# Kernel optimization log

Measured on AMD Instinct MI355X. Metric: run time of the kernel, lower is better.

The kernel has to match this reference:

```python
import jax, jax.numpy as jnp
import numpy as np

N = 50000      # num_nodes
E = 1000000    # graph edges
EP = 400000    # pos/neg link-pred edges
H = 128        # hidden_dim
C = 768        # chemical_dim
L = 2          # num GCN layers


def setup_inputs() -> dict:
    key = jax.random.key(0)
    ks = jax.random.split(key, 12)
    edge_index = jax.random.randint(ks[0], (2, E), 0, N)
    chemistry = jax.random.normal(ks[1], (N, C), jnp.float32)
    pos_edge = jax.random.randint(ks[2], (EP, 2), 0, N)
    neg_edge = jax.random.randint(ks[3], (EP, 2), 0, N)
    smiles_mask = jax.random.uniform(ks[4], (N,), jnp.float32)
    node_emb = jax.random.normal(ks[5], (N, H), jnp.float32) * 0.1
    conv_w = jax.random.normal(ks[6], (L, H, H), jnp.float32) / np.sqrt(H)
    conv_b = jnp.zeros((L, H), jnp.float32)
    chem_w = jax.random.normal(ks[7], (C, H), jnp.float32) / np.sqrt(C)
    chem_b = jnp.zeros((H,), jnp.float32)
    dec_w1 = jax.random.normal(ks[8], (2 * H, H), jnp.float32) / np.sqrt(2 * H)
    dec_b1 = jnp.zeros((H,), jnp.float32)
    dec_w2 = jax.random.normal(ks[9], (H, 1), jnp.float32) / np.sqrt(H)
    dec_b2 = jnp.zeros((1,), jnp.float32)
    return dict(edge_index=edge_index, chemistry=chemistry, pos_edge=pos_edge,
                neg_edge=neg_edge, smiles_mask=smiles_mask, node_emb=node_emb,
                conv_w=conv_w, conv_b=conv_b, chem_w=chem_w, chem_b=chem_b,
                dec_w1=dec_w1, dec_b1=dec_b1, dec_w2=dec_w2, dec_b2=dec_b2)


def reference(edge_index, chemistry, pos_edge, neg_edge, smiles_mask, node_emb,
              conv_w, conv_b, chem_w, chem_b, dec_w1, dec_b1, dec_w2, dec_b2):
    row, col = edge_index[0], edge_index[1]  # src -> dst
    # GCN symmetric normalization (add_self_loops=False)
    deg = jax.ops.segment_sum(jnp.ones((E,), jnp.float32), col, num_segments=N)
    dinv = jnp.where(deg > 0, 1.0 / jnp.sqrt(jnp.maximum(deg, 1.0)), 0.0)
    norm = dinv[row] * dinv[col]  # [E]

    # Encoder: structure-only GCN over learned node embeddings
    z = node_emb
    for l in range(L):
        h = z @ conv_w[l]                       # [N,H]
        msg = h[row] * norm[:, None]            # gather [E,H]
        agg = jax.ops.segment_sum(msg, col, num_segments=N)  # scatter-add
        z = jax.nn.relu(agg + conv_b[l])

    # Chemistry projection, masked by smiles validity
    c = jax.nn.relu(chemistry @ chem_w + chem_b) * smiles_mask[:, None]  # [N,H]

    def decode(edges):
        src, dst = edges[:, 0], edges[:, 1]
        f = jnp.concatenate([z[src] * z[dst], c[src] * c[dst]], axis=-1)  # [Ep,2H]
        hmid = jax.nn.relu(f @ dec_w1 + dec_b1)
        return (hmid @ dec_w2 + dec_b2)[:, 0]

    return decode(pos_edge), decode(neg_edge)
```

## Files before the change

### kernel.cpp

```cpp
#include <hip/hip_runtime.h>
#include <hip/hip_bf16.h>

#define NN 50000
#define NE 1000000
#define NEP 400000
#define HD 128
#define CD 768
#define NB_SCAN 196
#define CKS 24

typedef __attribute__((ext_vector_type(8))) short bf16x8;
typedef __attribute__((ext_vector_type(4))) float f32x4;

__device__ __forceinline__ ushort f2bf(float x) {
    unsigned u = __float_as_uint(x);
    u += 0x7FFF + ((u >> 16) & 1);
    return (ushort)(u >> 16);
}
__device__ __forceinline__ float bf2f(ushort b) {
    return __uint_as_float(((unsigned)b) << 16);
}
__device__ __forceinline__ unsigned pk2bf(float a, float b) {
    __hip_bfloat162 h = __float22bfloat162_rn(make_float2(a, b));
    return *(unsigned*)&h;
}
__device__ __forceinline__ bf16x8 pack8(float4 a0, float4 a1) {
    union { unsigned u[4]; bf16x8 v; } r;
    r.u[0] = pk2bf(a0.x, a0.y);
    r.u[1] = pk2bf(a0.z, a0.w);
    r.u[2] = pk2bf(a1.x, a1.y);
    r.u[3] = pk2bf(a1.z, a1.w);
    return r.v;
}

__global__ __launch_bounds__(256) void count_kernel(const int* __restrict__ col,
                                                    int* __restrict__ cnt) {
    int i = blockIdx.x * 256 + threadIdx.x;
    if (i < NE) atomicAdd(&cnt[col[i]], 1);
}

__global__ __launch_bounds__(256) void dinv_kernel(const int* __restrict__ cnt,
                                                   float* __restrict__ dinv) {
    int i = blockIdx.x * 256 + threadIdx.x;
    if (i < NN) {
        int d = cnt[i];
        dinv[i] = (d > 0) ? 1.0f / sqrtf((float)d) : 0.0f;
    }
}

__global__ __launch_bounds__(256) void scan1_kernel(const int* __restrict__ cnt,
                                                    int* __restrict__ partial,
                                                    int* __restrict__ bsum) {
    __shared__ int s[256];
    int i = blockIdx.x * 256 + threadIdx.x;
    int v = (i < NN) ? cnt[i] : 0;
    s[threadIdx.x] = v;
    __syncthreads();
    for (int o = 1; o < 256; o <<= 1) {
        int t = (threadIdx.x >= o) ? s[threadIdx.x - o] : 0;
        __syncthreads();
        s[threadIdx.x] += t;
        __syncthreads();
    }
    if (i < NN) partial[i] = s[threadIdx.x] - v;
    if (threadIdx.x == 255) bsum[blockIdx.x] = s[255];
}

__global__ __launch_bounds__(256) void scan2_kernel(int* __restrict__ bsum) {
    __shared__ int s[256];
    int v = (threadIdx.x < NB_SCAN) ? bsum[threadIdx.x] : 0;
    s[threadIdx.x] = v;
    __syncthreads();
    for (int o = 1; o < 256; o <<= 1) {
        int t = (threadIdx.x >= o) ? s[threadIdx.x - o] : 0;
        __syncthreads();
        s[threadIdx.x] += t;
        __syncthreads();
    }
    if (threadIdx.x < NB_SCAN) bsum[threadIdx.x] = s[threadIdx.x] - v;
}

__global__ __launch_bounds__(256) void scan3_kernel(const int* __restrict__ partial,
                                                    const int* __restrict__ bsum,
                                                    int* __restrict__ off,
                                                    int* __restrict__ cursor) {
    int i = blockIdx.x * 256 + threadIdx.x;
    if (i < NN) {
        int o = partial[i] + bsum[blockIdx.x];
        off[i] = o;
        cursor[i] = o;
    }
}

__global__ __launch_bounds__(256) void fill_kernel(const int* __restrict__ row,
                                                   const int* __restrict__ col,
                                                   const float* __restrict__ dinv,
                                                   int* __restrict__ cursor,
                                                   int* __restrict__ csr_idx,
                                                   float* __restrict__ csr_w) {
    int e = blockIdx.x * 256 + threadIdx.x;
    if (e < NE) {
        int c = col[e], r = row[e];
        int slot = atomicAdd(&cursor[c], 1);
        csr_idx[slot] = r;
        csr_w[slot] = dinv[r];
    }
}

__global__ __launch_bounds__(256) void wfrag_kernel(const float* __restrict__ w,
                                                    ushort* __restrict__ wf) {
    int tid = blockIdx.x * 256 + threadIdx.x;
    int ks = tid >> 9, nt = (tid >> 6) & 7, l = tid & 63;
    int kbase = ks * 32 + ((l >> 4) << 3);
    int colq = nt * 16 + (l & 15);
    ushort r[8];
#pragma unroll
    for (int j = 0; j < 8; ++j) r[j] = f2bf(w[(size_t)(kbase + j) * HD + colq]);
    *(uint4*)&wf[(size_t)tid * 8] = *(uint4*)r;
}

__global__ __launch_bounds__(256) void matmul_kernel(const float* __restrict__ A,
                                                     const float* __restrict__ W,
                                                     ushort* __restrict__ outb,
                                                     int nrows) {
    __shared__ float Alds[64][64];
    __shared__ float Wlds[64][128];
    const int t = threadIdx.x;
    const int tcol = t & 31, trow = t >> 5;
    const int rowBase = blockIdx.x * 64;

    float4 acc[8];
#pragma unroll
    for (int r = 0; r < 8; ++r) acc[r] = make_float4(0.f, 0.f, 0.f, 0.f);

    for (int kc = 0; kc < HD; kc += 64) {
#pragma unroll
        for (int it = 0; it < 4; ++it) {
            int li = t + it * 256;
            int r = li >> 4, d4 = li & 15;
            int grow = rowBase + r;
            float4 v = make_float4(0.f, 0.f, 0.f, 0.f);
            if (grow < nrows) v = *(const float4*)&A[(size_t)grow * HD + kc + d4 * 4];
            ((float4*)&Alds[0][0])[li] = v;
        }
#pragma unroll
        for (int it = 0; it < 8; ++it) {
            int li = t + it * 256;
            ((float4*)&Wlds[0][0])[li] = ((const float4*)W)[(size_t)kc * 32 + li];
        }
        __syncthreads();
#pragma unroll
        for (int kk = 0; kk < 64; kk += 2) {
            float4 w0 = *(const float4*)&Wlds[kk][tcol * 4];
            float4 w1 = *(const float4*)&Wlds[kk + 1][tcol * 4];
#pragma unroll
            for (int r = 0; r < 8; ++r) {
                float2 a = *(const float2*)&Alds[trow * 8 + r][kk];
                acc[r].x = fmaf(a.x, w0.x, fmaf(a.y, w1.x, acc[r].x));
                acc[r].y = fmaf(a.x, w0.y, fmaf(a.y, w1.y, acc[r].y));
                acc[r].z = fmaf(a.x, w0.z, fmaf(a.y, w1.z, acc[r].z));
                acc[r].w = fmaf(a.x, w0.w, fmaf(a.y, w1.w, acc[r].w));
            }
        }
        __syncthreads();
    }
#pragma unroll
    for (int r = 0; r < 8; ++r) {
        int grow = rowBase + trow * 8 + r;
        if (grow < nrows) {
            uint2 pk;
            pk.x = pk2bf(acc[r].x, acc[r].y);
            pk.y = pk2bf(acc[r].z, acc[r].w);
            *(uint2*)&outb[(size_t)grow * HD + tcol * 4] = pk;
        }
    }
}

__global__ __launch_bounds__(256) void chem_mfma_kernel(const float* __restrict__ chem,
                                                        const ushort* __restrict__ wcf,
                                                        const float* __restrict__ bias,
                                                        const float* __restrict__ mask,
                                                        ushort* __restrict__ cb) {
    __shared__ float At[64][40];
    const int t = threadIdx.x;
    const int w = t >> 6, lane = t & 63;
    const int rowBase = blockIdx.x * 64;
    const int nt0 = w * 2;

    f32x4 acc[4][2] = {};

    for (int ks = 0; ks < CKS; ++ks) {
        __syncthreads();
#pragma unroll
        for (int i = 0; i < 2; ++i) {
            int li = t + i * 256;
            int r = li >> 3, c4 = li & 7;
            int grow = rowBase + r;
            float4 v = make_float4(0.f, 0.f, 0.f, 0.f);
            if (grow < NN) v = *(const float4*)&chem[(size_t)grow * CD + ks * 32 + c4 * 4];
            *(float4*)&At[r][c4 * 4] = v;
        }
        __syncthreads();
        bf16x8 bf0 = ((const bf16x8*)wcf)[(ks * 8 + nt0) * 64 + lane];
        bf16x8 bf1 = ((const bf16x8*)wcf)[(ks * 8 + nt0 + 1) * 64 + lane];
#pragma unroll
        for (int mt = 0; mt < 4; ++mt) {
            int row = mt * 16 + (lane & 15);
            float4 a0 = *(const float4*)&At[row][(lane >> 4) * 8];
            float4 a1 = *(const float4*)&At[row][(lane >> 4) * 8 + 4];
            bf16x8 af = pack8(a0, a1);
            acc[mt][0] = __builtin_amdgcn_mfma_f32_16x16x32_bf16(af, bf0, acc[mt][0], 0, 0, 0);
            acc[mt][1] = __builtin_amdgcn_mfma_f32_16x16x32_bf16(af, bf1, acc[mt][1], 0, 0, 0);
        }
    }

    const int c0 = lane & 15, rq = lane >> 4;
    float bb0 = bias[nt0 * 16 + c0];
    float bb1 = bias[nt0 * 16 + 16 + c0];
#pragma unroll
    for (int mt = 0; mt < 4; ++mt) {
#pragma unroll
        for (int reg = 0; reg < 4; ++reg) {
            int grow = rowBase + mt * 16 + rq * 4 + reg;
            if (grow < NN) {
                float m = mask[grow];
                cb[(size_t)grow * HD + nt0 * 16 + c0] = f2bf(fmaxf(acc[mt][0][reg] + bb0, 0.f) * m);
                cb[(size_t)grow * HD + nt0 * 16 + 16 + c0] = f2bf(fmaxf(acc[mt][1][reg] + bb1, 0.f) * m);
            }
        }
    }
}

template <bool BF16OUT>
__global__ __launch_bounds__(256) void gather_kernel(const int* __restrict__ off,
                                                     const int* __restrict__ cnt,
                                                     const int* __restrict__ csr_idx,
                                                     const float* __restrict__ csr_w,
                                                     const float* __restrict__ dinv,
                                                     const ushort* __restrict__ h,
                                                     const float* __restrict__ bias,
                                                     float* __restrict__ z,
                                                     ushort* __restrict__ zb) {
    int v = blockIdx.x * 4 + (threadIdx.x >> 6);
    if (v >= NN) return;
    int lane = threadIdx.x & 63;
    int s = off[v];
    int e = s + cnt[v];
    float accx = 0.f, accy = 0.f;
    for (; s + 3 < e; s += 4) {
        int r0 = csr_idx[s], r1 = csr_idx[s + 1], r2 = csr_idx[s + 2], r3 = csr_idx[s + 3];
        float w0 = csr_w[s], w1 = csr_w[s + 1], w2 = csr_w[s + 2], w3 = csr_w[s + 3];
        unsigned u0 = *(const unsigned*)&h[(size_t)r0 * HD + lane * 2];
        unsigned u1 = *(const unsigned*)&h[(size_t)r1 * HD + lane * 2];
        unsigned u2 = *(const unsigned*)&h[(size_t)r2 * HD + lane * 2];
        unsigned u3 = *(const unsigned*)&h[(size_t)r3 * HD + lane * 2];
        accx = fmaf(bf2f((ushort)u0), w0, accx); accy = fmaf(bf2f((ushort)(u0 >> 16)), w0, accy);
        accx = fmaf(bf2f((ushort)u1), w1, accx); accy = fmaf(bf2f((ushort)(u1 >> 16)), w1, accy);
        accx = fmaf(bf2f((ushort)u2), w2, accx); accy = fmaf(bf2f((ushort)(u2 >> 16)), w2, accy);
        accx = fmaf(bf2f((ushort)u3), w3, accx); accy = fmaf(bf2f((ushort)(u3 >> 16)), w3, accy);
    }
    for (; s < e; ++s) {
        int r0 = csr_idx[s];
        float w0 = csr_w[s];
        unsigned u0 = *(const unsigned*)&h[(size_t)r0 * HD + lane * 2];
        accx = fmaf(bf2f((ushort)u0), w0, accx); accy = fmaf(bf2f((ushort)(u0 >> 16)), w0, accy);
    }
    float dv = dinv[v];
    float2 b = *(const float2*)&bias[lane * 2];
    float ox = fmaxf(fmaf(accx, dv, b.x), 0.f);
    float oy = fmaxf(fmaf(accy, dv, b.y), 0.f);
    if (BF16OUT) {
        *(unsigned*)&zb[(size_t)v * HD + lane * 2] = pk2bf(ox, oy);
    } else {
        float2 o; o.x = ox; o.y = oy;
        *(float2*)&z[(size_t)v * HD + lane * 2] = o;
    }
}

__global__ __launch_bounds__(256) void decode_mfma_kernel(const int* __restrict__ pos_edge,
                                                          const int* __restrict__ neg_edge,
                                                          const ushort* __restrict__ zb,
                                                          const ushort* __restrict__ cb,
                                                          const ushort* __restrict__ w1f,
                                                          const float* __restrict__ b1,
                                                          const float* __restrict__ w2,
                                                          const float* __restrict__ b2,
                                                          float* __restrict__ out) {
    __shared__ ushort Flds[8 * 4 * 64 * 8];
    __shared__ int sEdge[128];
    __shared__ float part[4][64];
    const int t = threadIdx.x;
    const int w = t >> 6, lane = t & 63;
    const int bid = blockIdx.x;
    const bool isPos = bid < (NEP / 64);
    const int* edges = isPos ? pos_edge : neg_edge;
    const int ebase = (isPos ? bid : bid - NEP / 64) * 64;
    float* op = out + (isPos ? 0 : NEP);

    if (t < 128) sEdge[t] = edges[(size_t)ebase * 2 + t];
    __syncthreads();

    const int seg = lane & 15, esub = lane >> 4;
#pragma unroll
    for (int it = 0; it < 8; ++it) {
        int e = ((it & 3) << 4) | (w << 2) | esub;
        int half = it >> 2;
        const ushort* src = half ? cb : zb;
        int s = sEdge[2 * e], dd = sEdge[2 * e + 1];
        uint4 av = *(const uint4*)&src[(size_t)s * HD + seg * 8];
        uint4 bv = *(const uint4*)&src[(size_t)dd * HD + seg * 8];
        const ushort* ap = (const ushort*)&av;
        const ushort* bp = (const ushort*)&bv;
        uint4 res;
        res.x = pk2bf(bf2f(ap[0]) * bf2f(bp[0]), bf2f(ap[1]) * bf2f(bp[1]));
        res.y = pk2bf(bf2f(ap[2]) * bf2f(bp[2]), bf2f(ap[3]) * bf2f(bp[3]));
        res.z = pk2bf(bf2f(ap[4]) * bf2f(bp[4]), bf2f(ap[5]) * bf2f(bp[5]));
        res.w = pk2bf(bf2f(ap[6]) * bf2f(bp[6]), bf2f(ap[7]) * bf2f(bp[7]));
        int ks = half * 4 + (seg >> 2);
        int mt = it & 3;
        int fl = (e & 15) | ((seg & 3) << 4);
        int idx = (((ks * 4 + mt) * 64) + fl) ^ ((ks & 1) << 2);
        ((uint4*)Flds)[idx] = res;
    }
    __syncthreads();

    f32x4 acc[4][2] = {};
    const int nt0 = w * 2;
#pragma unroll
    for (int ks = 0; ks < 8; ++ks) {
        bf16x8 bf0 = ((const bf16x8*)w1f)[(ks * 8 + nt0) * 64 + lane];
        bf16x8 bf1 = ((const bf16x8*)w1f)[(ks * 8 + nt0 + 1) * 64 + lane];
#pragma unroll
        for (int mt = 0; mt < 4; ++mt) {
            bf16x8 af = ((const bf16x8*)Flds)[((ks * 4 + mt) * 64) + (lane ^ ((ks & 1) << 2))];
            acc[mt][0] = __builtin_amdgcn_mfma_f32_16x16x32_bf16(af, bf0, acc[mt][0], 0, 0, 0);
            acc[mt][1] = __builtin_amdgcn_mfma_f32_16x16x32_bf16(af, bf1, acc[mt][1], 0, 0, 0);
        }
    }

    const int c0 = lane & 15, rq = lane >> 4;
    float b1v0 = b1[nt0 * 16 + c0], b1v1 = b1[nt0 * 16 + 16 + c0];
    float w2v0 = w2[nt0 * 16 + c0], w2v1 = w2[nt0 * 16 + 16 + c0];
#pragma unroll
    for (int mt = 0; mt < 4; ++mt) {
#pragma unroll
        for (int reg = 0; reg < 4; ++reg) {
            float h0 = fmaxf(acc[mt][0][reg] + b1v0, 0.f);
            float h1 = fmaxf(acc[mt][1][reg] + b1v1, 0.f);
            float p = fmaf(h0, w2v0, h1 * w2v1);
            p += __shfl_xor(p, 1);
            p += __shfl_xor(p, 2);
            p += __shfl_xor(p, 4);
            p += __shfl_xor(p, 8);
            if (c0 == 0) part[w][mt * 16 + rq * 4 + reg] = p;
        }
    }
    __syncthreads();
    if (t < 64) {
        op[ebase + t] = part[0][t] + part[1][t] + part[2][t] + part[3][t] + b2[0];
    }
}

extern "C" void kernel_launch(void* const* d_in, const int* in_sizes, int n_in,
                              void* d_out, int out_size, void* d_ws, size_t ws_size,
                              hipStream_t stream) {
    const int* edge_index = (const int*)d_in[0];
    const float* chemistry = (const float*)d_in[1];
    const int* pos_edge = (const int*)d_in[2];
    const int* neg_edge = (const int*)d_in[3];
    const float* smiles_mask = (const float*)d_in[4];
    const float* node_emb = (const float*)d_in[5];
    const float* conv_w = (const float*)d_in[6];
    const float* conv_b = (const float*)d_in[7];
    const float* chem_w = (const float*)d_in[8];
    const float* chem_b = (const float*)d_in[9];
    const float* dec_w1 = (const float*)d_in[10];
    const float* dec_b1 = (const float*)d_in[11];
    const float* dec_w2 = (const float*)d_in[12];
    const float* dec_b2 = (const float*)d_in[13];
    float* out = (float*)d_out;

    char* ws = (char*)d_ws;
    int* cnt = (int*)(ws + 0);
    float* dinv = (float*)(ws + 204800);
    int* partial = (int*)(ws + 409600);
    int* off = (int*)(ws + 614400);
    int* cursor = (int*)(ws + 819200);
    int* bsum = (int*)(ws + 1024000);
    int* csr_idx = (int*)(ws + 1048576);
    float* csr_w = (float*)(ws + 5242880);
    float* bufZ = (float*)(ws + 9437184);
    ushort* hb = (ushort*)(ws + 35037184);
    ushort* zb = (ushort*)(ws + 47837184);
    ushort* cb = (ushort*)(ws + 60637184);
    ushort* w1f = (ushort*)(ws + 73437184);
    ushort* wcf = (ushort*)(ws + 73502720);

    const int* e_row = edge_index;
    const int* e_col = edge_index + NE;

    hipMemsetAsync(cnt, 0, (size_t)NN * 4, stream);
    count_kernel<<<(NE + 255) / 256, 256, 0, stream>>>(e_col, cnt);
    dinv_kernel<<<(NN + 255) / 256, 256, 0, stream>>>(cnt, dinv);
    scan1_kernel<<<NB_SCAN, 256, 0, stream>>>(cnt, partial, bsum);
    scan2_kernel<<<1, 256, 0, stream>>>(bsum);
    scan3_kernel<<<NB_SCAN, 256, 0, stream>>>(partial, bsum, off, cursor);
    fill_kernel<<<(NE + 255) / 256, 256, 0, stream>>>(e_row, e_col, dinv, cursor, csr_idx, csr_w);
    wfrag_kernel<<<16, 256, 0, stream>>>(dec_w1, w1f);
    wfrag_kernel<<<48, 256, 0, stream>>>(chem_w, wcf);

    const int mmGrid = (NN + 63) / 64;
    const int gaGrid = (NN + 3) / 4;

    matmul_kernel<<<mmGrid, 256, 0, stream>>>(node_emb, conv_w, hb, NN);
    gather_kernel<false><<<gaGrid, 256, 0, stream>>>(off, cnt, csr_idx, csr_w, dinv, hb, conv_b, bufZ, nullptr);

    matmul_kernel<<<mmGrid, 256, 0, stream>>>(bufZ, conv_w + HD * HD, hb, NN);
    gather_kernel<true><<<gaGrid, 256, 0, stream>>>(off, cnt, csr_idx, csr_w, dinv, hb, conv_b + HD, nullptr, zb);

    chem_mfma_kernel<<<mmGrid, 256, 0, stream>>>(chemistry, wcf, chem_b, smiles_mask, cb);

    decode_mfma_kernel<<<2 * (NEP / 64), 256, 0, stream>>>(pos_edge, neg_edge, zb, cb, w1f,
                                                           dec_b1, dec_w2, dec_b2, out);
}
```

Measured before the change: 482.9 us.

## Interleave z and c features per node and use MFMA for GCN matmuls

Result: faster. 460.5 us (-4.6%).

```diff
diff --git a/kernel.cpp b/kernel.cpp
--- a/kernel.cpp
+++ b/kernel.cpp
@@ -7,7 +7,7 @@
 #define HD 128
 #define CD 768
 #define NB_SCAN 196
-#define CKS 24
+#define FSTR 256
 
 typedef __attribute__((ext_vector_type(8))) short bf16x8;
 typedef __attribute__((ext_vector_type(4))) float f32x4;
@@ -119,77 +119,23 @@
     *(uint4*)&wf[(size_t)tid * 8] = *(uint4*)r;
 }
 
-__global__ __launch_bounds__(256) void matmul_kernel(const float* __restrict__ A,
-                                                     const float* __restrict__ W,
-                                                     ushort* __restrict__ outb,
-                                                     int nrows) {
-    __shared__ float Alds[64][64];
-    __shared__ float Wlds[64][128];
-    const int t = threadIdx.x;
-    const int tcol = t & 31, trow = t >> 5;
-    const int rowBase = blockIdx.x * 64;
-
-    float4 acc[8];
-#pragma unroll
-    for (int r = 0; r < 8; ++r) acc[r] = make_float4(0.f, 0.f, 0.f, 0.f);
-
-    for (int kc = 0; kc < HD; kc += 64) {
-#pragma unroll
-        for (int it = 0; it < 4; ++it) {
-            int li = t + it * 256;
-            int r = li >> 4, d4 = li & 15;
-            int grow = rowBase + r;
-            float4 v = make_float4(0.f, 0.f, 0.f, 0.f);
-            if (grow < nrows) v = *(const float4*)&A[(size_t)grow * HD + kc + d4 * 4];
-            ((float4*)&Alds[0][0])[li] = v;
-        }
-#pragma unroll
-        for (int it = 0; it < 8; ++it) {
-            int li = t + it * 256;
-            ((float4*)&Wlds[0][0])[li] = ((const float4*)W)[(size_t)kc * 32 + li];
-        }
-        __syncthreads();
-#pragma unroll
-        for (int kk = 0; kk < 64; kk += 2) {
-            float4 w0 = *(const float4*)&Wlds[kk][tcol * 4];
-            float4 w1 = *(const float4*)&Wlds[kk + 1][tcol * 4];
-#pragma unroll
-            for (int r = 0; r < 8; ++r) {
-                float2 a = *(const float2*)&Alds[trow * 8 + r][kk];
-                acc[r].x = fmaf(a.x, w0.x, fmaf(a.y, w1.x, acc[r].x));
-                acc[r].y = fmaf(a.x, w0.y, fmaf(a.y, w1.y, acc[r].y));
-                acc[r].z = fmaf(a.x, w0.z, fmaf(a.y, w1.z, acc[r].z));
-                acc[r].w = fmaf(a.x, w0.w, fmaf(a.y, w1.w, acc[r].w));
-            }
-        }
-        __syncthreads();
-    }
-#pragma unroll
-    for (int r = 0; r < 8; ++r) {
-        int grow = rowBase + trow * 8 + r;
-        if (grow < nrows) {
-            uint2 pk;
-            pk.x = pk2bf(acc[r].x, acc[r].y);
-            pk.y = pk2bf(acc[r].z, acc[r].w);
-            *(uint2*)&outb[(size_t)grow * HD + tcol * 4] = pk;
-        }
-    }
-}
-
-__global__ __launch_bounds__(256) void chem_mfma_kernel(const float* __restrict__ chem,
-                                                        const ushort* __restrict__ wcf,
+template <int KS, bool EPI>
+__global__ __launch_bounds__(256) void feat_mfma_kernel(const float* __restrict__ A,
+                                                        const ushort* __restrict__ wf,
                                                         const float* __restrict__ bias,
                                                         const float* __restrict__ mask,
-                                                        ushort* __restrict__ cb) {
-    __shared__ float At[64][40];
+                                                        ushort* __restrict__ out,
+                                                        int ostride, int ooff) {
+    __shared__ float At[64][36];
     const int t = threadIdx.x;
     const int w = t >> 6, lane = t & 63;
     const int rowBase = blockIdx.x * 64;
     const int nt0 = w * 2;
+    const int K = KS * 32;
 
     f32x4 acc[4][2] = {};
 
-    for (int ks = 0; ks < CKS; ++ks) {
+    for (int ks = 0; ks < KS; ++ks) {
         __syncthreads();
 #pragma unroll
         for (int i = 0; i < 2; ++i) {
@@ -197,12 +143,12 @@
             int r = li >> 3, c4 = li & 7;
             int grow = rowBase + r;
             float4 v = make_float4(0.f, 0.f, 0.f, 0.f);
-            if (grow < NN) v = *(const float4*)&chem[(size_t)grow * CD + ks * 32 + c4 * 4];
+            if (grow < NN) v = *(const float4*)&A[(size_t)grow * K + ks * 32 + c4 * 4];
             *(float4*)&At[r][c4 * 4] = v;
         }
         __syncthreads();
-        bf16x8 bf0 = ((const bf16x8*)wcf)[(ks * 8 + nt0) * 64 + lane];
-        bf16x8 bf1 = ((const bf16x8*)wcf)[(ks * 8 + nt0 + 1) * 64 + lane];
+        bf16x8 bf0 = ((const bf16x8*)wf)[(ks * 8 + nt0) * 64 + lane];
+        bf16x8 bf1 = ((const bf16x8*)wf)[(ks * 8 + nt0 + 1) * 64 + lane];
 #pragma unroll
         for (int mt = 0; mt < 4; ++mt) {
             int row = mt * 16 + (lane & 15);
@@ -215,17 +161,22 @@
     }
 
     const int c0 = lane & 15, rq = lane >> 4;
-    float bb0 = bias[nt0 * 16 + c0];
-    float bb1 = bias[nt0 * 16 + 16 + c0];
+    float bb0 = EPI ? bias[nt0 * 16 + c0] : 0.f;
+    float bb1 = EPI ? bias[nt0 * 16 + 16 + c0] : 0.f;
 #pragma unroll
     for (int mt = 0; mt < 4; ++mt) {
 #pragma unroll
         for (int reg = 0; reg < 4; ++reg) {
             int grow = rowBase + mt * 16 + rq * 4 + reg;
             if (grow < NN) {
-                float m = mask[grow];
-                cb[(size_t)grow * HD + nt0 * 16 + c0] = f2bf(fmaxf(acc[mt][0][reg] + bb0, 0.f) * m);
-                cb[(size_t)grow * HD + nt0 * 16 + 16 + c0] = f2bf(fmaxf(acc[mt][1][reg] + bb1, 0.f) * m);
+                float v0 = acc[mt][0][reg], v1 = acc[mt][1][reg];
+                if (EPI) {
+                    float m = mask[grow];
+                    v0 = fmaxf(v0 + bb0, 0.f) * m;
+                    v1 = fmaxf(v1 + bb1, 0.f) * m;
+                }
+                out[(size_t)grow * ostride + ooff + nt0 * 16 + c0] = f2bf(v0);
+                out[(size_t)grow * ostride + ooff + nt0 * 16 + 16 + c0] = f2bf(v1);
             }
         }
     }
@@ -240,7 +191,8 @@
                                                      const ushort* __restrict__ h,
                                                      const float* __restrict__ bias,
                                                      float* __restrict__ z,
-                                                     ushort* __restrict__ zb) {
+                                                     ushort* __restrict__ zb,
+                                                     int ostride) {
     int v = blockIdx.x * 4 + (threadIdx.x >> 6);
     if (v >= NN) return;
     int lane = threadIdx.x & 63;
@@ -270,7 +222,7 @@
     float ox = fmaxf(fmaf(accx, dv, b.x), 0.f);
     float oy = fmaxf(fmaf(accy, dv, b.y), 0.f);
     if (BF16OUT) {
-        *(unsigned*)&zb[(size_t)v * HD + lane * 2] = pk2bf(ox, oy);
+        *(unsigned*)&zb[(size_t)v * ostride + lane * 2] = pk2bf(ox, oy);
     } else {
         float2 o; o.x = ox; o.y = oy;
         *(float2*)&z[(size_t)v * HD + lane * 2] = o;
@@ -279,8 +231,7 @@
 
 __global__ __launch_bounds__(256) void decode_mfma_kernel(const int* __restrict__ pos_edge,
                                                           const int* __restrict__ neg_edge,
-                                                          const ushort* __restrict__ zb,
-                                                          const ushort* __restrict__ cb,
+                                                          const ushort* __restrict__ feat,
                                                           const ushort* __restrict__ w1f,
                                                           const float* __restrict__ b1,
                                                           const float* __restrict__ w2,
@@ -300,15 +251,13 @@
     if (t < 128) sEdge[t] = edges[(size_t)ebase * 2 + t];
     __syncthreads();
 
-    const int seg = lane & 15, esub = lane >> 4;
+    const int seg = t & 31, eslot = t >> 5;
 #pragma unroll
     for (int it = 0; it < 8; ++it) {
-        int e = ((it & 3) << 4) | (w << 2) | esub;
-        int half = it >> 2;
-        const ushort* src = half ? cb : zb;
+        int e = it * 8 + eslot;
         int s = sEdge[2 * e], dd = sEdge[2 * e + 1];
-        uint4 av = *(const uint4*)&src[(size_t)s * HD + seg * 8];
-        uint4 bv = *(const uint4*)&src[(size_t)dd * HD + seg * 8];
+        uint4 av = *(const uint4*)&feat[(size_t)s * FSTR + seg * 8];
+        uint4 bv = *(const uint4*)&feat[(size_t)dd * FSTR + seg * 8];
         const ushort* ap = (const ushort*)&av;
         const ushort* bp = (const ushort*)&bv;
         uint4 res;
@@ -316,11 +265,11 @@
         res.y = pk2bf(bf2f(ap[2]) * bf2f(bp[2]), bf2f(ap[3]) * bf2f(bp[3]));
         res.z = pk2bf(bf2f(ap[4]) * bf2f(bp[4]), bf2f(ap[5]) * bf2f(bp[5]));
         res.w = pk2bf(bf2f(ap[6]) * bf2f(bp[6]), bf2f(ap[7]) * bf2f(bp[7]));
-        int ks = half * 4 + (seg >> 2);
-        int mt = it & 3;
+        int ks = seg >> 2;
+        int mt = e >> 4;
         int fl = (e & 15) | ((seg & 3) << 4);
-        int idx = (((ks * 4 + mt) * 64) + fl) ^ ((ks & 1) << 2);
-        ((uint4*)Flds)[idx] = res;
+        int swz = (seg & 3) | ((ks & 1) << 2);
+        ((uint4*)Flds)[(ks * 4 + mt) * 64 + (fl ^ swz)] = res;
     }
     __syncthreads();
 
@@ -330,9 +279,10 @@
     for (int ks = 0; ks < 8; ++ks) {
         bf16x8 bf0 = ((const bf16x8*)w1f)[(ks * 8 + nt0) * 64 + lane];
         bf16x8 bf1 = ((const bf16x8*)w1f)[(ks * 8 + nt0 + 1) * 64 + lane];
+        const int rswz = ((lane >> 4) & 3) | ((ks & 1) << 2);
 #pragma unroll
         for (int mt = 0; mt < 4; ++mt) {
-            bf16x8 af = ((const bf16x8*)Flds)[((ks * 4 + mt) * 64) + (lane ^ ((ks & 1) << 2))];
+            bf16x8 af = ((const bf16x8*)Flds)[(ks * 4 + mt) * 64 + (lane ^ rswz)];
             acc[mt][0] = __builtin_amdgcn_mfma_f32_16x16x32_bf16(af, bf0, acc[mt][0], 0, 0, 0);
             acc[mt][1] = __builtin_amdgcn_mfma_f32_16x16x32_bf16(af, bf1, acc[mt][1], 0, 0, 0);
         }
@@ -391,10 +341,11 @@
     float* csr_w = (float*)(ws + 5242880);
     float* bufZ = (float*)(ws + 9437184);
     ushort* hb = (ushort*)(ws + 35037184);
-    ushort* zb = (ushort*)(ws + 47837184);
-    ushort* cb = (ushort*)(ws + 60637184);
+    ushort* feat = (ushort*)(ws + 47837184);
     ushort* w1f = (ushort*)(ws + 73437184);
     ushort* wcf = (ushort*)(ws + 73502720);
+    ushort* wc0f = (ushort*)(ws + 73699328);
+    ushort* wc1f = (ushort*)(ws + 73732096);
 
     const int* e_row = edge_index;
     const int* e_col = edge_index + NE;
@@ -408,18 +359,20 @@
     fill_kernel<<<(NE + 255) / 256, 256, 0, stream>>>(e_row, e_col, dinv, cursor, csr_idx, csr_w);
     wfrag_kernel<<<16, 256, 0, stream>>>(dec_w1, w1f);
     wfrag_kernel<<<48, 256, 0, stream>>>(chem_w, wcf);
+    wfrag_kernel<<<8, 256, 0, stream>>>(conv_w, wc0f);
+    wfrag_kernel<<<8, 256, 0, stream>>>(conv_w + HD * HD, wc1f);
 
     const int mmGrid = (NN + 63) / 64;
     const int gaGrid = (NN + 3) / 4;
 
-    matmul_kernel<<<mmGrid, 256, 0, stream>>>(node_emb, conv_w, hb, NN);
-    gather_kernel<false><<<gaGrid, 256, 0, stream>>>(off, cnt, csr_idx, csr_w, dinv, hb, conv_b, bufZ, nullptr);
-
-    matmul_kernel<<<mmGrid, 256, 0, stream>>>(bufZ, conv_w + HD * HD, hb, NN);
-    gather_kernel<true><<<gaGrid, 256, 0, stream>>>(off, cnt, csr_idx, csr_w, dinv, hb, conv_b + HD, nullptr, zb);
-
-    chem_mfma_kernel<<<mmGrid, 256, 0, stream>>>(chemistry, wcf, chem_b, smiles_mask, cb);
-
-    decode_mfma_kernel<<<2 * (NEP / 64), 256, 0, stream>>>(pos_edge, neg_edge, zb, cb, w1f,
+    feat_mfma_kernel<4, false><<<mmGrid, 256, 0, stream>>>(node_emb, wc0f, nullptr, nullptr, hb, HD, 0);
+    gather_kernel<false><<<gaGrid, 256, 0, stream>>>(off, cnt, csr_idx, csr_w, dinv, hb, conv_b, bufZ, nullptr, 0);
+
+    feat_mfma_kernel<4, false><<<mmGrid, 256, 0, stream>>>(bufZ, wc1f, nullptr, nullptr, hb, HD, 0);
+    gather_kernel<true><<<gaGrid, 256, 0, stream>>>(off, cnt, csr_idx, csr_w, dinv, hb, conv_b + HD, nullptr, feat, FSTR);
+
+    feat_mfma_kernel<24, true><<<mmGrid, 256, 0, stream>>>(chemistry, wcf, chem_b, smiles_mask, feat, FSTR, HD);
+
+    decode_mfma_kernel<<<2 * (NEP / 64), 256, 0, stream>>>(pos_edge, neg_edge, feat, w1f,
                                                            dec_b1, dec_w2, dec_b2, out);
 }
```
